# Kernel tuning notes

Hardware: AMD Instinct MI355X
Metric: run time of the kernel (lower is better)

The kernel has to match this reference:

```python
import jax, jax.numpy as jnp
import numpy as np

B, S, D = 4, 4096, 256
UNITS = 256
NRF = 256  # n_random_features (must equal units for the score matmul)


def setup_inputs() -> dict:
    key = jax.random.key(0)
    ks = jax.random.split(key, 10)
    s = 1.0 / np.sqrt(D)
    return {
        "query": jax.random.normal(ks[0], (B, S, D), jnp.float32),
        "value": jax.random.normal(ks[1], (B, S, D), jnp.float32),
        "Wq": jax.random.normal(ks[2], (D, UNITS), jnp.float32) * s,
        "bq": jnp.zeros((UNITS,), jnp.float32),
        "Wk": jax.random.normal(ks[3], (D, UNITS), jnp.float32) * s,
        "bk": jnp.zeros((UNITS,), jnp.float32),
        "Wv": jax.random.normal(ks[4], (D, UNITS), jnp.float32) * s,
        "bv": jnp.zeros((UNITS,), jnp.float32),
        # random-feature map params (non-trainable in original, init 'random_normal' ~ stddev 0.05)
        "Wr": jax.random.normal(ks[5], (UNITS, NRF), jnp.float32) * 0.05,
        "br": jax.random.normal(ks[6], (NRF,), jnp.float32) * 0.05,
    }


def reference(query, value, Wq, bq, Wk, bk, Wv, bv, Wr, br):
    # Dense projections
    Q = jnp.einsum("bsd,du->bsu", query, Wq) + bq   # [B,S,U]
    K = jnp.einsum("bsd,du->bsu", value, Wk) + bk   # [B,S,U]
    V = jnp.einsum("bsd,du->bsu", value, Wv) + bv   # [B,S,U]
    # random-feature kernel map on K
    K_hat = jnp.cos(jnp.einsum("bsu,ur->bsr", K, Wr) + br)  # [B,S,R]
    # attention: Q @ K_hat^T -> softmax -> @ V
    scores = jnp.einsum("bqr,bkr->bqk", Q, K_hat)    # [B,S,S]
    probs = jax.nn.softmax(scores, axis=-1)
    return jnp.einsum("bqk,bku->bqu", probs, V)      # [B,S,U]
```

## Files before the change

kernel.cpp:

```cpp
#include <hip/hip_runtime.h>
#include <hip/hip_bf16.h>

typedef _Float16 f16;
typedef _Float16 f16x8 __attribute__((ext_vector_type(8)));
typedef _Float16 f16x4 __attribute__((ext_vector_type(4)));
typedef float f32x4 __attribute__((ext_vector_type(4)));
typedef float f32x16 __attribute__((ext_vector_type(16)));

#define MFMA1632(a, b, c) __builtin_amdgcn_mfma_f32_16x16x32_f16(a, b, c, 0, 0, 0)
#define MFMA3216(a, b, c) __builtin_amdgcn_mfma_f32_32x32x16_f16(a, b, c, 0, 0, 0)

#define GLL16(g, l)                                                        \
    __builtin_amdgcn_global_load_lds(                                      \
        (const __attribute__((address_space(1))) void*)(g),                \
        (__attribute__((address_space(3))) void*)(l), 16, 0, 0)

static constexpr int S  = 4096;
static constexpr int NB = 4;

__global__ void wconv4_kernel(const float* __restrict__ W0, const float* __restrict__ W1,
                              const float* __restrict__ W2, const float* __restrict__ W3,
                              f16* __restrict__ T0, f16* __restrict__ T1,
                              f16* __restrict__ T2, f16* __restrict__ T3) {
    int j = blockIdx.x >> 8;
    int k = blockIdx.x & 255;
    int n = threadIdx.x;
    const float* W = (j == 0) ? W0 : (j == 1) ? W1 : (j == 2) ? W2 : W3;
    f16*         T = (j == 0) ? T0 : (j == 1) ? T1 : (j == 2) ? T2 : T3;
    T[n * 256 + k] = (f16)W[k * 256 + n];
}

template <int ASRC, int OMODE>
__global__ __launch_bounds__(256) void proj_kernel(
    const float* __restrict__ Af, const f16* __restrict__ Ah,
    const f16* __restrict__ Wt, const float* __restrict__ bias,
    f16* __restrict__ O)
{
    int mbase = blockIdx.x * 32;
    int tid = threadIdx.x;
    int w = tid >> 6, l = tid & 63;
    int lr = l & 15, lg = l >> 4;
    int nbase = w * 64;

    f32x4 acc[2][4];
#pragma unroll
    for (int mf = 0; mf < 2; ++mf)
#pragma unroll
        for (int nf = 0; nf < 4; ++nf) acc[mf][nf] = f32x4{0.f, 0.f, 0.f, 0.f};

#pragma unroll
    for (int ks = 0; ks < 8; ++ks) {
        int kof = ks * 32 + lg * 8;
        f16x8 a[2], b[4];
#pragma unroll
        for (int mf = 0; mf < 2; ++mf) {
            int row = mbase + mf * 16 + lr;
            if (ASRC == 0) {
                const float4* p = (const float4*)(Af + row * 256 + kof);
                float4 x0 = p[0], x1 = p[1];
                f16x8 t;
                t[0] = (f16)x0.x; t[1] = (f16)x0.y; t[2] = (f16)x0.z; t[3] = (f16)x0.w;
                t[4] = (f16)x1.x; t[5] = (f16)x1.y; t[6] = (f16)x1.z; t[7] = (f16)x1.w;
                a[mf] = t;
            } else {
                a[mf] = *(const f16x8*)(Ah + row * 256 + kof);
            }
        }
#pragma unroll
        for (int nf = 0; nf < 4; ++nf) {
            int col = nbase + nf * 16 + lr;
            b[nf] = *(const f16x8*)(Wt + col * 256 + kof);
        }
#pragma unroll
        for (int mf = 0; mf < 2; ++mf)
#pragma unroll
            for (int nf = 0; nf < 4; ++nf)
                acc[mf][nf] = MFMA1632(a[mf], b[nf], acc[mf][nf]);
    }

#pragma unroll
    for (int mf = 0; mf < 2; ++mf) {
#pragma unroll
        for (int nf = 0; nf < 4; ++nf) {
            int col = nbase + nf * 16 + lr;
            float bv = bias[col];
#pragma unroll
            for (int r = 0; r < 4; ++r) {
                int row = mbase + mf * 16 + lg * 4 + r;
                float x = acc[mf][nf][r] + bv;
                if (OMODE == 1) x = cosf(x);
                O[row * 256 + col] = (f16)x;
            }
        }
    }
}

__global__ __launch_bounds__(512) void kvproj_kernel(
    const float* __restrict__ Af,
    const f16* __restrict__ WkT, const f16* __restrict__ WvT,
    const float* __restrict__ bk, const float* __restrict__ bv,
    f16* __restrict__ Kf, f16* __restrict__ VtF)
{
    int mbase = blockIdx.x * 32;
    int tid = threadIdx.x;
    int w = tid >> 6, l = tid & 63;
    int lr = l & 15, lg = l >> 4;
    int path = w >> 2;
    int nbase = (w & 3) * 64;
    const f16* Wt = path ? WvT : WkT;
    const float* bias = path ? bv : bk;

    f32x4 acc[2][4];
#pragma unroll
    for (int mf = 0; mf < 2; ++mf)
#pragma unroll
        for (int nf = 0; nf < 4; ++nf) acc[mf][nf] = f32x4{0.f, 0.f, 0.f, 0.f};

#pragma unroll
    for (int ks = 0; ks < 8; ++ks) {
        int kof = ks * 32 + lg * 8;
        f16x8 a[2], b[4];
#pragma unroll
        for (int mf = 0; mf < 2; ++mf) {
            int row = mbase + mf * 16 + lr;
            const float4* p = (const float4*)(Af + row * 256 + kof);
            float4 x0 = p[0], x1 = p[1];
            f16x8 t;
            t[0] = (f16)x0.x; t[1] = (f16)x0.y; t[2] = (f16)x0.z; t[3] = (f16)x0.w;
            t[4] = (f16)x1.x; t[5] = (f16)x1.y; t[6] = (f16)x1.z; t[7] = (f16)x1.w;
            a[mf] = t;
        }
#pragma unroll
        for (int nf = 0; nf < 4; ++nf) {
            int col = nbase + nf * 16 + lr;
            b[nf] = *(const f16x8*)(Wt + col * 256 + kof);
        }
#pragma unroll
        for (int mf = 0; mf < 2; ++mf)
#pragma unroll
            for (int nf = 0; nf < 4; ++nf)
                acc[mf][nf] = MFMA1632(a[mf], b[nf], acc[mf][nf]);
    }

#pragma unroll
    for (int mf = 0; mf < 2; ++mf) {
#pragma unroll
        for (int nf = 0; nf < 4; ++nf) {
            int col = nbase + nf * 16 + lr;
            float bv2 = bias[col];
            if (path == 0) {
#pragma unroll
                for (int r = 0; r < 4; ++r) {
                    int row = mbase + mf * 16 + lg * 4 + r;
                    Kf[row * 256 + col] = (f16)(acc[mf][nf][r] + bv2);
                }
            } else {
                int bi = mbase >> 12;
                int s  = (mbase & (S - 1)) + mf * 16 + lg * 4;
                f16x4 v;
#pragma unroll
                for (int r = 0; r < 4; ++r) v[r] = (f16)(acc[mf][nf][r] + bv2);
                *(f16x4*)(VtF + ((bi * 256 + col) * S + s)) = v;
            }
        }
    }
}

__global__ __launch_bounds__(512, 2) void attn_kernel(
    const f16* __restrict__ Qf, const f16* __restrict__ Hf,
    const f16* __restrict__ Vt, float* __restrict__ Out)
{
    __shared__ f16 KhS[128 * 256];
    __shared__ f16 VtS2[128 * 256];
    __shared__ f16 PSh2[32 * 256];
    __shared__ float auxF[2][4][32];
    __shared__ float auxT[2][32];
    __shared__ float auxC[2][32];
    __shared__ int flagLds;

    int bid = blockIdx.x;
    int b   = (bid >> 1) & 3;
    int qi  = ((bid >> 3) << 1) | (bid & 1);
    int qbase = qi * 64;

    int tid = threadIdx.x;
    int w  = tid >> 6, l = tid & 63;
    int qh = w >> 2;
    int kg = w & 3;
    int lm = l & 31;
    int h  = l >> 5;

    const f16* Hbase = Hf + (size_t)b * S * 256;
    const f16* Vbase = Vt + (size_t)b * 256 * S;

    f16x8 qf[16];
    {
        const f16* qp = Qf + (size_t)(b * S + qbase + qh * 32 + lm) * 256 + h * 8;
#pragma unroll
        for (int s = 0; s < 16; ++s) qf[s] = *(const f16x8*)(qp + s * 16);
    }

    f32x16 oac0, oac1;
#pragma unroll
    for (int i = 0; i < 16; ++i) { oac0[i] = 0.f; oac1[i] = 0.f; }
    float mrun = -1e30f, lsum = 0.f;

    if (tid == 0) flagLds = 0;

#pragma unroll
    for (int i = 0; i < 8; ++i) {
        int c = i * 512 + tid;
        int row = c >> 5, ch = c & 31;
        GLL16(Hbase + (size_t)row * 256 + ((ch ^ (row & 31)) * 8),
              KhS + (size_t)(i * 4096 + w * 512));
    }
#pragma unroll
    for (int i = 0; i < 8; ++i) {
        int j   = i * 64 + l;
        int prv = j >> 5, pc = j & 31;
        int kap = (w * 16 + prv) & 31;
        int lc  = pc ^ kap;
        int d   = w * 32 + prv * 2 + (lc >> 4);
        GLL16(Vbase + (size_t)d * S + ((lc & 15) * 8),
              VtS2 + (size_t)(w * 4096 + i * 512));
    }
    __syncthreads();

    const int NT = S / 128;
    for (int t = 0; t < NT; ++t) {
        int kt = t * 128;

        f32x16 s0, s1;
#pragma unroll
        for (int i = 0; i < 16; ++i) { s0[i] = 0.f; s1[i] = 0.f; }
        {
            const f16* kb = KhS + (size_t)(kg * 32 + lm) * 256;
            __builtin_amdgcn_s_setprio(1);
#pragma unroll
            for (int s = 0; s < 16; s += 2) {
                f16x8 ka0 = *(const f16x8*)(kb + ((2 * s + h) ^ lm) * 8);
                f16x8 ka1 = *(const f16x8*)(kb + ((2 * s + 2 + h) ^ lm) * 8);
                s0 = MFMA3216(ka0, qf[s], s0);
                s1 = MFMA3216(ka1, qf[s + 1], s1);
            }
            __builtin_amdgcn_s_setprio(0);
        }
        f32x16 sc;
#pragma unroll
        for (int i = 0; i < 16; ++i) sc[i] = s0[i] + s1[i];

        int need = 0;
#pragma unroll
        for (int i = 0; i < 16; ++i) need |= (sc[i] > mrun + 8.f) ? 1 : 0;
        if (__any(need)) { if (l == 0) flagLds = 1; }
        __syncthreads();

        if (t + 1 < NT) {
#pragma unroll
            for (int i = 0; i < 8; ++i) {
                int c = i * 512 + tid;
                int row = c >> 5, ch = c & 31;
                GLL16(Hbase + (size_t)(kt + 128 + row) * 256 + ((ch ^ (row & 31)) * 8),
                      KhS + (size_t)(i * 4096 + w * 512));
            }
        }

        if (flagLds) {
            float mx = sc[0];
#pragma unroll
            for (int i = 1; i < 16; ++i) mx = fmaxf(mx, sc[i]);
            mx = fmaxf(mx, __shfl_xor(mx, 32));
            if (l < 32) auxF[qh][kg][lm] = mx;
            __syncthreads();
            float mnew = fmaxf(fmaxf(auxF[qh][0][lm], auxF[qh][1][lm]),
                               fmaxf(auxF[qh][2][lm], auxF[qh][3][lm]));
            mnew = fmaxf(mrun, mnew);
            float corr = __expf(mrun - mnew);
            lsum *= corr;
            if (kg == 0 && l < 32) auxT[qh][lm] = corr;
            mrun = mnew;
            if (tid == 0) flagLds = 0;
            __syncthreads();
#pragma unroll
            for (int i = 0; i < 16; ++i) {
                int cr = (i & 3) + 8 * (i >> 2) + 4 * h;
                oac0[i] *= auxT[0][cr];
                oac1[i] *= auxT[1][cr];
            }
        }

        {
            int pr = qh * 16 + (lm >> 1);
            f16* pw = PSh2 + (size_t)pr * 256 + 4 * h;
            int pcb = (lm & 1) * 16;
#pragma unroll
            for (int b4 = 0; b4 < 4; ++b4) {
                float p0 = __expf(sc[b4 * 4 + 0] - mrun);
                float p1 = __expf(sc[b4 * 4 + 1] - mrun);
                float p2 = __expf(sc[b4 * 4 + 2] - mrun);
                float p3 = __expf(sc[b4 * 4 + 3] - mrun);
                lsum += (p0 + p1) + (p2 + p3);
                f16x4 pv;
                pv[0] = (f16)p0; pv[1] = (f16)p1; pv[2] = (f16)p2; pv[3] = (f16)p3;
                *(f16x4*)(pw + ((pcb + 4 * kg + b4) ^ pr) * 8) = pv;
            }
        }

        __syncthreads();

        {
            const f16* pb0 = PSh2 + (size_t)(lm >> 1) * 256;
            const f16* pb1 = PSh2 + (size_t)(16 + (lm >> 1)) * 256;
            const f16* vb  = VtS2 + (size_t)(w * 16 + (lm >> 1)) * 256;
            int kpa0 = (lm >> 1);
            int kpa1 = 16 + (lm >> 1);
            int kv   = (w * 16 + (lm >> 1)) & 31;
            int bq0  = (lm & 1) * 16;
            __builtin_amdgcn_s_setprio(1);
#pragma unroll
            for (int s = 0; s < 8; ++s) {
                int lc = bq0 + 2 * s + h;
                f16x8 pa0 = *(const f16x8*)(pb0 + (lc ^ kpa0) * 8);
                f16x8 pa1 = *(const f16x8*)(pb1 + (lc ^ kpa1) * 8);
                f16x8 vv  = *(const f16x8*)(vb  + (lc ^ kv) * 8);
                oac0 = MFMA3216(pa0, vv, oac0);
                oac1 = MFMA3216(pa1, vv, oac1);
            }
            __builtin_amdgcn_s_setprio(0);
        }

        if (t + 1 < NT) {
#pragma unroll
            for (int i = 0; i < 8; ++i) {
                int j   = i * 64 + l;
                int prv = j >> 5, pc = j & 31;
                int kap = (w * 16 + prv) & 31;
                int lc  = pc ^ kap;
                int d   = w * 32 + prv * 2 + (lc >> 4);
                GLL16(Vbase + (size_t)d * S + (kt + 128) + ((lc & 15) * 8),
                      VtS2 + (size_t)(w * 4096 + i * 512));
            }
        }
    }

    lsum += __shfl_xor(lsum, 32);
    if (l < 32) auxF[qh][kg][lm] = lsum;
    __syncthreads();
    if (kg == 0 && l < 32) {
        float dsum = auxF[qh][0][lm] + auxF[qh][1][lm] +
                     auxF[qh][2][lm] + auxF[qh][3][lm];
        auxC[qh][lm] = 1.0f / dsum;
    }
    __syncthreads();

    float* Ob = Out + (size_t)(b * S + qbase) * 256 + w * 32 + lm;
#pragma unroll
    for (int i = 0; i < 16; ++i) {
        int cr = (i & 3) + 8 * (i >> 2) + 4 * h;
        Ob[(size_t)cr * 256]        = oac0[i] * auxC[0][cr];
        Ob[(size_t)(32 + cr) * 256] = oac1[i] * auxC[1][cr];
    }
}

extern "C" void kernel_launch(void* const* d_in, const int* in_sizes, int n_in,
                              void* d_out, int out_size, void* d_ws, size_t ws_size,
                              hipStream_t stream)
{
    const float* query = (const float*)d_in[0];
    const float* value = (const float*)d_in[1];
    const float* Wq    = (const float*)d_in[2];
    const float* bq    = (const float*)d_in[3];
    const float* Wk    = (const float*)d_in[4];
    const float* bk    = (const float*)d_in[5];
    const float* Wv    = (const float*)d_in[6];
    const float* bv    = (const float*)d_in[7];
    const float* Wr    = (const float*)d_in[8];
    const float* br    = (const float*)d_in[9];
    float* out = (float*)d_out;

    char* ws = (char*)d_ws;
    size_t off = 0;
    auto alloc = [&](size_t bytes) -> char* {
        char* p = ws + off;
        off += (bytes + 255) & ~(size_t)255;
        return p;
    };
    f16* WqT = (f16*)alloc((size_t)65536 * 2);
    f16* WkT = (f16*)alloc((size_t)65536 * 2);
    f16* WvT = (f16*)alloc((size_t)65536 * 2);
    f16* WrT = (f16*)alloc((size_t)65536 * 2);
    f16* Qf  = (f16*)alloc((size_t)NB * S * 256 * 2);
    f16* Kf  = (f16*)alloc((size_t)NB * S * 256 * 2);
    f16* Hf  = (f16*)alloc((size_t)NB * S * 256 * 2);
    f16* VtF = (f16*)alloc((size_t)NB * S * 256 * 2);
    (void)ws_size; (void)in_sizes; (void)n_in; (void)out_size;

    wconv4_kernel<<<1024, 256, 0, stream>>>(Wq, Wk, Wv, Wr, WqT, WkT, WvT, WrT);

    proj_kernel<0, 0><<<512, 256, 0, stream>>>(query, nullptr, WqT, bq, Qf);
    kvproj_kernel<<<512, 512, 0, stream>>>(value, WkT, WvT, bk, bv, Kf, VtF);
    proj_kernel<1, 1><<<512, 256, 0, stream>>>(nullptr, Kf, WrT, br, Hf);

    attn_kernel<<<256, 512, 0, stream>>>(Qf, Hf, VtF, out);
}
```

Baseline: 173.5 us.

## Fuse random-feature projection into KV kernel and rework attention V/P LDS layout

Measured after the change: 165.0 us. 4.9% less time.

```diff
diff --git a/kernel.cpp b/kernel.cpp
--- a/kernel.cpp
+++ b/kernel.cpp
@@ -30,11 +30,9 @@
     T[n * 256 + k] = (f16)W[k * 256 + n];
 }
 
-template <int ASRC, int OMODE>
-__global__ __launch_bounds__(256) void proj_kernel(
-    const float* __restrict__ Af, const f16* __restrict__ Ah,
-    const f16* __restrict__ Wt, const float* __restrict__ bias,
-    f16* __restrict__ O)
+__global__ __launch_bounds__(256) void qproj_kernel(
+    const float* __restrict__ Af, const f16* __restrict__ Wt,
+    const float* __restrict__ bias, f16* __restrict__ O)
 {
     int mbase = blockIdx.x * 32;
     int tid = threadIdx.x;
@@ -55,16 +53,12 @@
 #pragma unroll
         for (int mf = 0; mf < 2; ++mf) {
             int row = mbase + mf * 16 + lr;
-            if (ASRC == 0) {
-                const float4* p = (const float4*)(Af + row * 256 + kof);
-                float4 x0 = p[0], x1 = p[1];
-                f16x8 t;
-                t[0] = (f16)x0.x; t[1] = (f16)x0.y; t[2] = (f16)x0.z; t[3] = (f16)x0.w;
-                t[4] = (f16)x1.x; t[5] = (f16)x1.y; t[6] = (f16)x1.z; t[7] = (f16)x1.w;
-                a[mf] = t;
-            } else {
-                a[mf] = *(const f16x8*)(Ah + row * 256 + kof);
-            }
+            const float4* p = (const float4*)(Af + row * 256 + kof);
+            float4 x0 = p[0], x1 = p[1];
+            f16x8 t;
+            t[0] = (f16)x0.x; t[1] = (f16)x0.y; t[2] = (f16)x0.z; t[3] = (f16)x0.w;
+            t[4] = (f16)x1.x; t[5] = (f16)x1.y; t[6] = (f16)x1.z; t[7] = (f16)x1.w;
+            a[mf] = t;
         }
 #pragma unroll
         for (int nf = 0; nf < 4; ++nf) {
@@ -87,20 +81,22 @@
 #pragma unroll
             for (int r = 0; r < 4; ++r) {
                 int row = mbase + mf * 16 + lg * 4 + r;
-                float x = acc[mf][nf][r] + bv;
-                if (OMODE == 1) x = cosf(x);
-                O[row * 256 + col] = (f16)x;
+                O[row * 256 + col] = (f16)(acc[mf][nf][r] + bv);
             }
         }
     }
 }
 
-__global__ __launch_bounds__(512) void kvproj_kernel(
+__global__ __launch_bounds__(512) void kvhproj_kernel(
     const float* __restrict__ Af,
     const f16* __restrict__ WkT, const f16* __restrict__ WvT,
+    const f16* __restrict__ WrT,
     const float* __restrict__ bk, const float* __restrict__ bv,
-    f16* __restrict__ Kf, f16* __restrict__ VtF)
+    const float* __restrict__ br,
+    f16* __restrict__ Hf, f16* __restrict__ VtF)
 {
+    __shared__ f16 KS[32][264];
+
     int mbase = blockIdx.x * 32;
     int tid = threadIdx.x;
     int w = tid >> 6, l = tid & 63;
@@ -150,10 +146,8 @@
             float bv2 = bias[col];
             if (path == 0) {
 #pragma unroll
-                for (int r = 0; r < 4; ++r) {
-                    int row = mbase + mf * 16 + lg * 4 + r;
-                    Kf[row * 256 + col] = (f16)(acc[mf][nf][r] + bv2);
-                }
+                for (int r = 0; r < 4; ++r)
+                    KS[mf * 16 + lg * 4 + r][col] = (f16)(acc[mf][nf][r] + bv2);
             } else {
                 int bi = mbase >> 12;
                 int s  = (mbase & (S - 1)) + mf * 16 + lg * 4;
@@ -161,6 +155,46 @@
 #pragma unroll
                 for (int r = 0; r < 4; ++r) v[r] = (f16)(acc[mf][nf][r] + bv2);
                 *(f16x4*)(VtF + ((bi * 256 + col) * S + s)) = v;
+            }
+        }
+    }
+    __syncthreads();
+
+    f32x4 acc2[2][2];
+#pragma unroll
+    for (int mf = 0; mf < 2; ++mf)
+#pragma unroll
+        for (int nf = 0; nf < 2; ++nf) acc2[mf][nf] = f32x4{0.f, 0.f, 0.f, 0.f};
+
+#pragma unroll
+    for (int ks = 0; ks < 8; ++ks) {
+        int kof = ks * 32 + lg * 8;
+        f16x8 a[2], b[2];
+#pragma unroll
+        for (int mf = 0; mf < 2; ++mf)
+            a[mf] = *(const f16x8*)&KS[mf * 16 + lr][kof];
+#pragma unroll
+        for (int nf = 0; nf < 2; ++nf) {
+            int col = w * 32 + nf * 16 + lr;
+            b[nf] = *(const f16x8*)(WrT + col * 256 + kof);
+        }
+#pragma unroll
+        for (int mf = 0; mf < 2; ++mf)
+#pragma unroll
+            for (int nf = 0; nf < 2; ++nf)
+                acc2[mf][nf] = MFMA1632(a[mf], b[nf], acc2[mf][nf]);
+    }
+
+#pragma unroll
+    for (int mf = 0; mf < 2; ++mf) {
+#pragma unroll
+        for (int nf = 0; nf < 2; ++nf) {
+            int col = w * 32 + nf * 16 + lr;
+            float bv2 = br[col];
+#pragma unroll
+            for (int r = 0; r < 4; ++r) {
+                int row = mbase + mf * 16 + lg * 4 + r;
+                Hf[row * 256 + col] = (f16)cosf(acc2[mf][nf][r] + bv2);
             }
         }
     }
@@ -171,8 +205,8 @@
     const f16* __restrict__ Vt, float* __restrict__ Out)
 {
     __shared__ f16 KhS[128 * 256];
-    __shared__ f16 VtS2[128 * 256];
-    __shared__ f16 PSh2[32 * 256];
+    __shared__ f16 VtS[256 * 128];
+    __shared__ f16 PSh[64 * 128];
     __shared__ float auxF[2][4][32];
     __shared__ float auxT[2][32];
     __shared__ float auxC[2][32];
@@ -216,13 +250,10 @@
     }
 #pragma unroll
     for (int i = 0; i < 8; ++i) {
-        int j   = i * 64 + l;
-        int prv = j >> 5, pc = j & 31;
-        int kap = (w * 16 + prv) & 31;
-        int lc  = pc ^ kap;
-        int d   = w * 32 + prv * 2 + (lc >> 4);
-        GLL16(Vbase + (size_t)d * S + ((lc & 15) * 8),
-              VtS2 + (size_t)(w * 4096 + i * 512));
+        int d  = w * 32 + i * 4 + (l >> 4);
+        int cp = l & 15;
+        GLL16(Vbase + (size_t)d * S + ((cp ^ (d & 15)) * 8),
+              VtS + (size_t)(w * 4096 + i * 512));
     }
     __syncthreads();
 
@@ -290,9 +321,8 @@
         }
 
         {
-            int pr = qh * 16 + (lm >> 1);
-            f16* pw = PSh2 + (size_t)pr * 256 + 4 * h;
-            int pcb = (lm & 1) * 16;
+            f16* pw = PSh + (size_t)(qh * 32 + lm) * 128;
+            int key = lm & 15;
 #pragma unroll
             for (int b4 = 0; b4 < 4; ++b4) {
                 float p0 = __expf(sc[b4 * 4 + 0] - mrun);
@@ -302,27 +332,25 @@
                 lsum += (p0 + p1) + (p2 + p3);
                 f16x4 pv;
                 pv[0] = (f16)p0; pv[1] = (f16)p1; pv[2] = (f16)p2; pv[3] = (f16)p3;
-                *(f16x4*)(pw + ((pcb + 4 * kg + b4) ^ pr) * 8) = pv;
-            }
-        }
-
-        __syncthreads();
+                *(f16x4*)(pw + ((4 * kg + b4) ^ key) * 8 + 4 * h) = pv;
+            }
+        }
+
+        asm volatile("s_waitcnt lgkmcnt(0)" ::: "memory");
+        __builtin_amdgcn_s_barrier();
 
         {
-            const f16* pb0 = PSh2 + (size_t)(lm >> 1) * 256;
-            const f16* pb1 = PSh2 + (size_t)(16 + (lm >> 1)) * 256;
-            const f16* vb  = VtS2 + (size_t)(w * 16 + (lm >> 1)) * 256;
-            int kpa0 = (lm >> 1);
-            int kpa1 = 16 + (lm >> 1);
-            int kv   = (w * 16 + (lm >> 1)) & 31;
-            int bq0  = (lm & 1) * 16;
+            const f16* pb0 = PSh + (size_t)lm * 128;
+            const f16* pb1 = PSh + (size_t)(32 + lm) * 128;
+            const f16* vb  = VtS + (size_t)(w * 32 + lm) * 128;
+            int kp = lm & 15;
             __builtin_amdgcn_s_setprio(1);
 #pragma unroll
             for (int s = 0; s < 8; ++s) {
-                int lc = bq0 + 2 * s + h;
-                f16x8 pa0 = *(const f16x8*)(pb0 + (lc ^ kpa0) * 8);
-                f16x8 pa1 = *(const f16x8*)(pb1 + (lc ^ kpa1) * 8);
-                f16x8 vv  = *(const f16x8*)(vb  + (lc ^ kv) * 8);
+                int lc = 2 * s + h;
+                f16x8 pa0 = *(const f16x8*)(pb0 + (lc ^ kp) * 8);
+                f16x8 pa1 = *(const f16x8*)(pb1 + (lc ^ kp) * 8);
+                f16x8 vv  = *(const f16x8*)(vb  + (lc ^ kp) * 8);
                 oac0 = MFMA3216(pa0, vv, oac0);
                 oac1 = MFMA3216(pa1, vv, oac1);
             }
@@ -332,15 +360,15 @@
         if (t + 1 < NT) {
 #pragma unroll
             for (int i = 0; i < 8; ++i) {
-                int j   = i * 64 + l;
-                int prv = j >> 5, pc = j & 31;
-                int kap = (w * 16 + prv) & 31;
-                int lc  = pc ^ kap;
-                int d   = w * 32 + prv * 2 + (lc >> 4);
-                GLL16(Vbase + (size_t)d * S + (kt + 128) + ((lc & 15) * 8),
-                      VtS2 + (size_t)(w * 4096 + i * 512));
-            }
-        }
+                int d  = w * 32 + i * 4 + (l >> 4);
+                int cp = l & 15;
+                GLL16(Vbase + (size_t)d * S + (kt + 128) + ((cp ^ (d & 15)) * 8),
+                      VtS + (size_t)(w * 4096 + i * 512));
+            }
+        }
+
+        asm volatile("s_waitcnt vmcnt(8)" ::: "memory");
+        __builtin_amdgcn_s_barrier();
     }
 
     lsum += __shfl_xor(lsum, 32);
@@ -390,16 +418,14 @@
     f16* WvT = (f16*)alloc((size_t)65536 * 2);
     f16* WrT = (f16*)alloc((size_t)65536 * 2);
     f16* Qf  = (f16*)alloc((size_t)NB * S * 256 * 2);
-    f16* Kf  = (f16*)alloc((size_t)NB * S * 256 * 2);
     f16* Hf  = (f16*)alloc((size_t)NB * S * 256 * 2);
     f16* VtF = (f16*)alloc((size_t)NB * S * 256 * 2);
     (void)ws_size; (void)in_sizes; (void)n_in; (void)out_size;
 
     wconv4_kernel<<<1024, 256, 0, stream>>>(Wq, Wk, Wv, Wr, WqT, WkT, WvT, WrT);
 
-    proj_kernel<0, 0><<<512, 256, 0, stream>>>(query, nullptr, WqT, bq, Qf);
-    kvproj_kernel<<<512, 512, 0, stream>>>(value, WkT, WvT, bk, bv, Kf, VtF);
-    proj_kernel<1, 1><<<512, 256, 0, stream>>>(nullptr, Kf, WrT, br, Hf);
+    qproj_kernel<<<512, 256, 0, stream>>>(query, WqT, bq, Qf);
+    kvhproj_kernel<<<512, 512, 0, stream>>>(value, WkT, WvT, WrT, bk, bv, br, Hf, VtF);
 
     attn_kernel<<<256, 512, 0, stream>>>(Qf, Hf, VtF, out);
 }
```
